# Kernel tuning notes

Hardware: AMD Instinct MI355X
Metric: run time of the kernel (lower is better)

The kernel has to match this reference:

```python
import jax, jax.numpy as jnp
import numpy as np

N, E, G = 100000, 300000, 4096
ND, ED, H, ZI, ZS, NE, L = 64, 16, 256, 128, 128, 8, 3
LAMBDA_GRL = 1.0


def setup_inputs() -> dict:
    key = jax.random.key(0)
    ks = iter(jax.random.split(key, 64))
    def nrm(shape, scale=0.05):
        return jax.random.normal(next(ks), shape, jnp.float32) * scale
    inp = {
        'x': jax.random.normal(next(ks), (N, ND), jnp.float32),
        'edge_index': jax.random.randint(next(ks), (2, E), 0, N),
        'edge_attr': jax.random.normal(next(ks), (E, ED), jnp.float32),
        'batch': jnp.sort(jax.random.randint(next(ks), (N,), 0, G)),
        'node_W': nrm((ND, H)), 'node_b': nrm((H,)),
        'conv_eps': jnp.zeros((L,), jnp.float32),
        'edge_W': nrm((L, ED, H)), 'edge_b': nrm((L, H)),
        'mlp_W1': nrm((L, H, H)), 'mlp_b1': nrm((L, H)),
        'mlp_W2': nrm((L, H, H)), 'mlp_b2': nrm((L, H)),
        'gn_w': jnp.ones((L, H), jnp.float32), 'gn_b': jnp.zeros((L, H), jnp.float32),
        'gn_ms': jnp.ones((L, H), jnp.float32),
        'finv_W1': nrm((H, ZI)), 'finv_b1': nrm((ZI,)),
        'finv_W2': nrm((ZI, ZI)), 'finv_b2': nrm((ZI,)),
        'fspu_W1': nrm((H, ZS)), 'fspu_b1': nrm((ZS,)),
        'fspu_W2': nrm((ZS, ZS)), 'fspu_b2': nrm((ZS,)),
        'pred_W1': nrm((ZI, ZI)), 'pred_b1': nrm((ZI,)),
        'pred_W2': nrm((ZI, 1)), 'pred_b2': nrm((1,)),
        'adv_W1': nrm((ZI, ZI)), 'adv_b1': nrm((ZI,)),
        'adv_W2': nrm((ZI, NE)), 'adv_b2': nrm((NE,)),
    }
    return inp


def _mlp2(h, W1, b1, W2, b2):
    return jax.nn.relu(h @ W1 + b1) @ W2 + b2


def reference(x, edge_index, edge_attr, batch, node_W, node_b, conv_eps,
              edge_W, edge_b, mlp_W1, mlp_b1, mlp_W2, mlp_b2,
              gn_w, gn_b, gn_ms,
              finv_W1, finv_b1, finv_W2, finv_b2,
              fspu_W1, fspu_b1, fspu_W2, fspu_b2,
              pred_W1, pred_b1, pred_W2, pred_b2,
              adv_W1, adv_b1, adv_W2, adv_b2):
    src, dst = edge_index[0], edge_index[1]
    cnt = jax.ops.segment_sum(jnp.ones((N, 1), jnp.float32), batch, num_segments=G)
    cnt = jnp.maximum(cnt, 1.0)
    h = x @ node_W + node_b  # [N,H]
    for l in range(L):
        # GINEConv: sum_j relu(x_j + lin(e_ij))
        e = edge_attr @ edge_W[l] + edge_b[l]            # [E,H]
        m = jax.nn.relu(h[src] + e)                      # [E,H]
        agg = jax.ops.segment_sum(m, dst, num_segments=N)
        h = _mlp2((1.0 + conv_eps[l]) * h + agg, mlp_W1[l], mlp_b1[l], mlp_W2[l], mlp_b2[l])
        # GraphNorm
        mean = jax.ops.segment_sum(h, batch, num_segments=G) / cnt  # [G,H]
        out = h - gn_ms[l] * mean[batch]
        var = jax.ops.segment_sum(out * out, batch, num_segments=G) / cnt
        h = out * jax.lax.rsqrt(var[batch] + 1e-5) * gn_w[l] + gn_b[l]
        h = jax.nn.relu(h)  # dropout is identity at eval
    hg = jax.ops.segment_sum(h, batch, num_segments=G) / cnt  # global_mean_pool [G,H]
    z_inv = _mlp2(hg, finv_W1, finv_b1, finv_W2, finv_b2)
    z_spu = _mlp2(hg, fspu_W1, fspu_b1, fspu_W2, fspu_b2)
    yhat = _mlp2(z_inv, pred_W1, pred_b1, pred_W2, pred_b2)[:, 0]
    # gradient reversal: identity fwd, -lambda on bwd
    grl = jax.lax.stop_gradient(z_inv) * (1.0 + LAMBDA_GRL) - LAMBDA_GRL * z_inv
    envhat = _mlp2(grl, adv_W1, adv_b1, adv_W2, adv_b2)
    return (hg, z_inv, z_spu, yhat, envhat)
```

## Files before the change

kernel.cpp:

```cpp
#include <hip/hip_runtime.h>
#include <hip/hip_bf16.h>

typedef __bf16 bf16_t;
typedef __bf16 bf16x8 __attribute__((ext_vector_type(8)));
typedef __bf16 bf16x4 __attribute__((ext_vector_type(4)));
typedef float  f32x4  __attribute__((ext_vector_type(4)));

static constexpr int N_NODES = 100000;
static constexpr int N_EDGES = 300000;
static constexpr int N_GRAPH = 4096;
static constexpr int H  = 256;
static constexpr int ND = 64;
static constexpr int ZIC = 128;
static constexpr int NE = 8;
static constexpr int SCAN_B = 1024;

__device__ __forceinline__ int clampi(int v, int lo, int hi) {
  return v < lo ? lo : (v > hi ? hi : v);
}

__device__ __forceinline__ void dma16(const bf16_t* g, bf16_t* lds_base) {
  __builtin_amdgcn_global_load_lds(
      (const __attribute__((address_space(1))) void*)g,
      (__attribute__((address_space(3))) void*)lds_base, 16, 0, 0);
}

__global__ void compute_starts_kernel(const int* __restrict__ batch,
                                      int* __restrict__ starts, int N, int G) {
  int i = blockIdx.x * blockDim.x + threadIdx.x;
  if (i >= N) return;
  int b = clampi(batch[i], 0, G - 1);
  if (i == 0) {
    for (int g = 0; g <= b; ++g) starts[g] = 0;
  } else {
    int p = clampi(batch[i - 1], 0, G - 1);
    for (int g = p + 1; g <= b; ++g) starts[g] = i;
  }
  if (i == N - 1) {
    for (int g = b + 1; g <= G; ++g) starts[g] = N;
  }
}

__global__ void zero2_kernel(int* __restrict__ a, int* __restrict__ b, int N) {
  int i = blockIdx.x * blockDim.x + threadIdx.x;
  if (i < N) { a[i] = 0; b[i] = 0; }
}

__global__ void count_deg_kernel(const int* __restrict__ dst, int* __restrict__ counts, int E, int N) {
  int e = blockIdx.x * blockDim.x + threadIdx.x;
  if (e < E) atomicAdd(&counts[clampi(dst[e], 0, N - 1)], 1);
}

__global__ __launch_bounds__(SCAN_B) void scan1_kernel(const int* __restrict__ counts,
                                                       int* __restrict__ offs,
                                                       int* __restrict__ bsum, int N) {
  __shared__ int tmp[SCAN_B];
  int i = blockIdx.x * SCAN_B + threadIdx.x;
  int v = (i < N) ? counts[i] : 0;
  tmp[threadIdx.x] = v;
  __syncthreads();
  for (int d = 1; d < SCAN_B; d <<= 1) {
    int t = (threadIdx.x >= d) ? tmp[threadIdx.x - d] : 0;
    __syncthreads();
    tmp[threadIdx.x] += t;
    __syncthreads();
  }
  if (i < N) offs[i + 1] = tmp[threadIdx.x];
  if (threadIdx.x == SCAN_B - 1) bsum[blockIdx.x] = tmp[SCAN_B - 1];
  if (i == 0) offs[0] = 0;
}

__global__ void scan2_kernel(int* __restrict__ bsum, int nblk) {
  if (blockIdx.x == 0 && threadIdx.x == 0) {
    int run = 0;
    for (int b = 0; b < nblk; ++b) { int v = bsum[b]; bsum[b] = run; run += v; }
  }
}

__global__ __launch_bounds__(SCAN_B) void scan3_kernel(int* __restrict__ offs,
                                                       const int* __restrict__ bsum, int N) {
  int i = blockIdx.x * SCAN_B + threadIdx.x;
  if (i < N) offs[i + 1] += bsum[blockIdx.x];
}

__global__ void fill_scatter_kernel(const int* __restrict__ src, const int* __restrict__ dst,
                                    const float* __restrict__ eattr,
                                    const int* __restrict__ offs, int* __restrict__ cursor,
                                    int* __restrict__ src_srt, bf16_t* __restrict__ eat16,
                                    int E, int N) {
  int e = blockIdx.x * blockDim.x + threadIdx.x;
  if (e >= E) return;
  int d = clampi(dst[e], 0, N - 1);
  int pos = offs[d] + atomicAdd(&cursor[d], 1);
  if ((unsigned)pos >= (unsigned)E) return;
  int s = src[e];
  src_srt[pos] = ((unsigned)s < (unsigned)N_NODES) ? s : 0;
  const float* ea = eattr + (size_t)e * 16;
  union { bf16_t b[16]; uint4 u[2]; } pk;
#pragma unroll
  for (int k = 0; k < 16; ++k) pk.b[k] = (bf16_t)ea[k];
  uint4* dst16 = (uint4*)(eat16 + ((size_t)pos << 4));
  dst16[0] = pk.u[0];
  dst16[1] = pk.u[1];
}

__global__ void build_ewt16_kernel(const float* __restrict__ edge_W,
                                   bf16_t* __restrict__ ewt) {
  int idx = blockIdx.x * blockDim.x + threadIdx.x;
  if (idx >= 3 * 256 * 16) return;
  int l = idx / (256 * 16);
  int rem = idx - l * 256 * 16;
  int n = rem >> 4, k = rem & 15;
  ewt[idx] = (bf16_t)edge_W[(size_t)l * 16 * 256 + k * 256 + n];
}

__global__ void transpose_kernel(const float* __restrict__ W,
                                 bf16_t* __restrict__ Wt, int K, int Nc,
                                 size_t srcStride, size_t dstStride) {
  __shared__ float tile[32][33];
  const float* Wz = W + (size_t)blockIdx.z * srcStride;
  bf16_t* Wtz = Wt + (size_t)blockIdx.z * dstStride;
  int n0 = blockIdx.x * 32, k0 = blockIdx.y * 32;
  int tx = threadIdx.x, ty = threadIdx.y;
  for (int i = ty; i < 32; i += 8)
    tile[i][tx] = Wz[(size_t)(k0 + i) * Nc + n0 + tx];
  __syncthreads();
  for (int i = ty; i < 32; i += 8)
    Wtz[(size_t)(n0 + i) * K + k0 + tx] = (bf16_t)tile[tx][i];
}

__device__ __forceinline__ void load8_to_lds(const bf16_t* p, bool valid, uint4* dst) {
  uint4 v = make_uint4(0u, 0u, 0u, 0u);
  if (valid) v = *(const uint4*)p;
  *dst = v;
}
__device__ __forceinline__ void load8_to_lds(const float* p, bool valid, uint4* dst) {
  float4 f0 = make_float4(0.f, 0.f, 0.f, 0.f), f1 = f0;
  if (valid) { f0 = *(const float4*)p; f1 = *(const float4*)(p + 4); }
  union { bf16_t b[8]; uint4 u; } pk;
  pk.b[0] = (bf16_t)f0.x; pk.b[1] = (bf16_t)f0.y;
  pk.b[2] = (bf16_t)f0.z; pk.b[3] = (bf16_t)f0.w;
  pk.b[4] = (bf16_t)f1.x; pk.b[5] = (bf16_t)f1.y;
  pk.b[6] = (bf16_t)f1.z; pk.b[7] = (bf16_t)f1.w;
  *dst = pk.u;
}

template<int K, bool RELU, bool OUTF32, typename TIN>
__global__ __launch_bounds__(256) void gemm128_kernel(
    const TIN* __restrict__ U, const bf16_t* __restrict__ Wt,
    const float* __restrict__ bias, void* __restrict__ Out, int M, int Nc) {
  constexpr int LDT = 72;
  __shared__ bf16_t Ut[128 * LDT];
  __shared__ bf16_t Wl[128 * LDT];
  const int m0 = blockIdx.x * 128;
  const int n0 = blockIdx.y * 128;
  const int t = threadIdx.x;
  const int lane = t & 63;
  const int wave = t >> 6;
  const int wm = (wave >> 1) * 64;
  const int wn = (wave & 1) * 64;
  const int srow = t >> 1;
  const int sk = (t & 1) * 32;
  const int lr = lane & 15;
  const int lq = lane >> 4;
  const bool aok = (m0 + srow) < M;
  f32x4 acc[4][4] = {};

  for (int k0 = 0; k0 < K; k0 += 64) {
    const TIN* up = U + (size_t)(m0 + srow) * K + k0 + sk;
    const bf16_t* wp = Wt + (size_t)(n0 + srow) * K + k0 + sk;
#pragma unroll
    for (int q = 0; q < 4; ++q) {
      load8_to_lds(up + q * 8, aok, (uint4*)&Ut[srow * LDT + sk + q * 8]);
      load8_to_lds(wp + q * 8, true, (uint4*)&Wl[srow * LDT + sk + q * 8]);
    }
    __syncthreads();
#pragma unroll
    for (int s = 0; s < 2; ++s) {
      bf16x8 a[4], b[4];
#pragma unroll
      for (int mt = 0; mt < 4; ++mt)
        a[mt] = *(const bf16x8*)(&Ut[(wm + mt * 16 + lr) * LDT + s * 32 + lq * 8]);
#pragma unroll
      for (int nt = 0; nt < 4; ++nt)
        b[nt] = *(const bf16x8*)(&Wl[(wn + nt * 16 + lr) * LDT + s * 32 + lq * 8]);
#pragma unroll
      for (int mt = 0; mt < 4; ++mt)
#pragma unroll
        for (int nt = 0; nt < 4; ++nt)
          acc[mt][nt] = __builtin_amdgcn_mfma_f32_16x16x32_bf16(
              a[mt], b[nt], acc[mt][nt], 0, 0, 0);
    }
    __syncthreads();
  }

#pragma unroll
  for (int mt = 0; mt < 4; ++mt)
#pragma unroll
    for (int nt = 0; nt < 4; ++nt) {
      int col = n0 + wn + nt * 16 + lr;
      float bcol = bias[col];
#pragma unroll
      for (int r = 0; r < 4; ++r) {
        int row = m0 + wm + mt * 16 + lq * 4 + r;
        if (row < M) {
          float vv = acc[mt][nt][r] + bcol;
          if (RELU) vv = vv > 0.f ? vv : 0.f;
          if (OUTF32) ((float*)Out)[(size_t)row * Nc + col] = vv;
          else        ((bf16_t*)Out)[(size_t)row * Nc + col] = (bf16_t)vv;
        }
      }
    }
}

template<int K, bool RELU, bool OUTF32, typename TIN>
__global__ __launch_bounds__(256) void gemm64_kernel(
    const TIN* __restrict__ U, const bf16_t* __restrict__ Wt,
    const float* __restrict__ bias, void* __restrict__ Out, int M, int Nc) {
  constexpr int LDT = 72;
  __shared__ bf16_t Ut[64 * LDT];
  __shared__ bf16_t Wl[64 * LDT];
  const int m0 = blockIdx.x * 64;
  const int n0 = blockIdx.y * 64;
  const int t = threadIdx.x;
  const int lane = t & 63;
  const int wave = t >> 6;
  const int wm = (wave >> 1) * 32;
  const int wn = (wave & 1) * 32;
  const int srow = t >> 2;
  const int sk = (t & 3) * 8;
  const int lr = lane & 15;
  const int lq = lane >> 4;
  const bool aok = (m0 + srow) < M;
  f32x4 acc[2][2] = {};

  for (int k0 = 0; k0 < K; k0 += 64) {
    const TIN* up = U + (size_t)(m0 + srow) * K + k0 + sk;
    const bf16_t* wp = Wt + (size_t)(n0 + srow) * K + k0 + sk;
    load8_to_lds(up,      aok, (uint4*)&Ut[srow * LDT + sk]);
    load8_to_lds(up + 32, aok, (uint4*)&Ut[srow * LDT + sk + 32]);
    load8_to_lds(wp,      true, (uint4*)&Wl[srow * LDT + sk]);
    load8_to_lds(wp + 32, true, (uint4*)&Wl[srow * LDT + sk + 32]);
    __syncthreads();
#pragma unroll
    for (int s = 0; s < 2; ++s) {
      bf16x8 a[2], b[2];
#pragma unroll
      for (int mt = 0; mt < 2; ++mt)
        a[mt] = *(const bf16x8*)(&Ut[(wm + mt * 16 + lr) * LDT + s * 32 + lq * 8]);
#pragma unroll
      for (int nt = 0; nt < 2; ++nt)
        b[nt] = *(const bf16x8*)(&Wl[(wn + nt * 16 + lr) * LDT + s * 32 + lq * 8]);
#pragma unroll
      for (int mt = 0; mt < 2; ++mt)
#pragma unroll
        for (int nt = 0; nt < 2; ++nt)
          acc[mt][nt] = __builtin_amdgcn_mfma_f32_16x16x32_bf16(
              a[mt], b[nt], acc[mt][nt], 0, 0, 0);
    }
    __syncthreads();
  }

#pragma unroll
  for (int mt = 0; mt < 2; ++mt)
#pragma unroll
    for (int nt = 0; nt < 2; ++nt) {
      int col = n0 + wn + nt * 16 + lr;
      float bcol = bias[col];
#pragma unroll
      for (int r = 0; r < 4; ++r) {
        int row = m0 + wm + mt * 16 + lq * 4 + r;
        if (row < M) {
          float vv = acc[mt][nt][r] + bcol;
          if (RELU) vv = vv > 0.f ? vv : 0.f;
          if (OUTF32) ((float*)Out)[(size_t)row * Nc + col] = vv;
          else        ((bf16_t*)Out)[(size_t)row * Nc + col] = (bf16_t)vv;
        }
      }
    }
}

template<int K, bool RELU, bool OUTF32>
__global__ __launch_bounds__(256) void gemm128_dma_kernel(
    const bf16_t* __restrict__ U, const bf16_t* __restrict__ Wt,
    const float* __restrict__ bias, void* __restrict__ Out, int M, int Nc) {
  __shared__ bf16_t Ut[128 * 64];
  __shared__ bf16_t Wl[128 * 64];
  const int t = threadIdx.x;
  const int lane = t & 63;
  const int wave = t >> 6;
  const int m0 = blockIdx.x * 128;
  const int n0 = blockIdx.y * 128;
  const int wm = (wave >> 1) * 64;
  const int wn = (wave & 1) * 64;
  const int lr = lane & 15;
  const int lq = lane >> 4;
  const int subrow = wave * 8 + (lane >> 3);
  const int lchunk = (lane & 7) ^ (lane >> 3);
  f32x4 acc[4][4] = {};

  for (int k0 = 0; k0 < K; k0 += 64) {
#pragma unroll
    for (int q = 0; q < 4; ++q) {
      const int row = q * 32 + subrow;
      int urow = m0 + row; if (urow >= M) urow = M - 1;
      dma16(U + (size_t)urow * K + k0 + lchunk * 8, &Ut[(q * 32 + wave * 8) * 64]);
      dma16(Wt + (size_t)(n0 + row) * K + k0 + lchunk * 8, &Wl[(q * 32 + wave * 8) * 64]);
    }
    __syncthreads();
#pragma unroll
    for (int s = 0; s < 2; ++s) {
      bf16x8 a[4], b[4];
#pragma unroll
      for (int mt = 0; mt < 4; ++mt)
        a[mt] = *(const bf16x8*)(&Ut[(wm + mt * 16 + lr) * 64 + (((s * 4 + lq) ^ (lr & 7)) << 3)]);
#pragma unroll
      for (int nt = 0; nt < 4; ++nt)
        b[nt] = *(const bf16x8*)(&Wl[(wn + nt * 16 + lr) * 64 + (((s * 4 + lq) ^ (lr & 7)) << 3)]);
#pragma unroll
      for (int mt = 0; mt < 4; ++mt)
#pragma unroll
        for (int nt = 0; nt < 4; ++nt)
          acc[mt][nt] = __builtin_amdgcn_mfma_f32_16x16x32_bf16(
              a[mt], b[nt], acc[mt][nt], 0, 0, 0);
    }
    __syncthreads();
  }

#pragma unroll
  for (int mt = 0; mt < 4; ++mt)
#pragma unroll
    for (int nt = 0; nt < 4; ++nt) {
      int col = n0 + wn + nt * 16 + lr;
      float bcol = bias[col];
#pragma unroll
      for (int r = 0; r < 4; ++r) {
        int row = m0 + wm + mt * 16 + lq * 4 + r;
        if (row < M) {
          float vv = acc[mt][nt][r] + bcol;
          if (RELU) vv = vv > 0.f ? vv : 0.f;
          if (OUTF32) ((float*)Out)[(size_t)row * Nc + col] = vv;
          else        ((bf16_t*)Out)[(size_t)row * Nc + col] = (bf16_t)vv;
        }
      }
    }
}

__global__ __launch_bounds__(256) void gine_gather_mfma_kernel(
    const bf16_t* __restrict__ h, const bf16_t* __restrict__ eat16,
    const int* __restrict__ src_sorted, const int* __restrict__ offs,
    const bf16_t* __restrict__ ewt, const float* __restrict__ eb,
    const float* __restrict__ eps_p, bf16_t* __restrict__ u) {
  constexpr int HP = H + 8;
  __shared__ bf16_t slin[2][16 * HP];
  const int t = threadIdx.x;
  const int wave = t >> 6;
  const int lane = t & 63;
  const int lr = lane & 15;
  const int lq = lane >> 4;
  const int lane4 = lane * 4;
  const int n0 = blockIdx.x * 4;
  const int nodeN = n0 + wave;

  bf16x4 hs = *(const bf16x4*)(h + (size_t)nodeN * H + lane4);

  bf16x8 bfrag[4];
#pragma unroll
  for (int nt = 0; nt < 4; ++nt) {
    bf16x8 bv = {};
    if (lq < 2)
      bv = *(const bf16x8*)(ewt + ((wave * 64 + nt * 16 + lr) << 4) + (lq << 3));
    bfrag[nt] = bv;
  }
  float ebv[4];
#pragma unroll
  for (int i = 0; i < 4; ++i) ebv[i] = eb[lane4 + i];

  int bs = offs[n0], be = offs[n0 + 4];
  bs = clampi(bs, 0, N_EDGES);
  be = clampi(be, bs, N_EDGES);
  int ns = offs[nodeN], ne = offs[nodeN + 1];
  ns = clampi(ns, bs, be);
  ne = clampi(ne, ns, be);

  float acc[4] = {0.f, 0.f, 0.f, 0.f};
  int parity = 0;

  for (int cb = bs; cb < be; cb += 16, parity ^= 1) {
    int arow = cb + lr;
    if (arow >= N_EDGES) arow = N_EDGES - 1;
    bf16x8 afrag = {};
    if (lq < 2)
      afrag = *(const bf16x8*)(eat16 + ((size_t)arow << 4) + (lq << 3));
    f32x4 c[4];
#pragma unroll
    for (int nt = 0; nt < 4; ++nt) {
      f32x4 z = {};
      c[nt] = __builtin_amdgcn_mfma_f32_16x16x32_bf16(afrag, bfrag[nt], z, 0, 0, 0);
    }
#pragma unroll
    for (int nt = 0; nt < 4; ++nt)
#pragma unroll
      for (int r = 0; r < 4; ++r)
        slin[parity][(lq * 4 + r) * HP + wave * 64 + nt * 16 + lr] = (bf16_t)c[nt][r];
    __syncthreads();
    int j0 = ns > cb ? ns : cb;
    int j1 = ne < cb + 16 ? ne : cb + 16;
    for (int jb = j0; jb < j1; jb += 4) {
      int sidx[4];
#pragma unroll
      for (int q = 0; q < 4; ++q) {
        int jj = jb + q; if (jj > j1 - 1) jj = j1 - 1;
        sidx[q] = src_sorted[jj];
      }
      bf16x4 hv[4];
#pragma unroll
      for (int q = 0; q < 4; ++q)
        hv[q] = *(const bf16x4*)(h + (size_t)sidx[q] * H + lane4);
#pragma unroll
      for (int q = 0; q < 4; ++q) {
        if (jb + q < j1) {
          bf16x4 lv = *(const bf16x4*)(&slin[parity][(jb + q - cb) * HP + lane4]);
#pragma unroll
          for (int i = 0; i < 4; ++i)
            acc[i] += fmaxf((float)hv[q][i] + (float)lv[i] + ebv[i], 0.f);
        }
      }
    }
  }

  const float sc = 1.0f + eps_p[0];
  union { bf16x4 v; uint2 b; } o;
#pragma unroll
  for (int i = 0; i < 4; ++i) o.v[i] = (bf16_t)(sc * (float)hs[i] + acc[i]);
  *(uint2*)(u + (size_t)nodeN * H + lane4) = o.b;
}

__global__ __launch_bounds__(64) void graphnorm_kernel(
    const bf16_t* __restrict__ v, bf16_t* __restrict__ hout,
    const int* __restrict__ starts,
    const float* __restrict__ w, const float* __restrict__ b,
    const float* __restrict__ ms, float* __restrict__ hg) {
  const int g = blockIdx.x;
  const int c0 = threadIdx.x * 4;
  int s = starts[g], e = starts[g + 1];
  s = clampi(s, 0, N_NODES);
  e = clampi(e, s, N_NODES);
  const float cnt = (float)((e - s) > 1 ? (e - s) : 1);
  float sx[4] = {0.f, 0.f, 0.f, 0.f}, sxx[4] = {0.f, 0.f, 0.f, 0.f};
  int i = s;
  for (; i + 4 <= e; i += 4) {
    bf16x4 xv[4];
#pragma unroll
    for (int q = 0; q < 4; ++q)
      xv[q] = *(const bf16x4*)(v + (size_t)(i + q) * H + c0);
#pragma unroll
    for (int q = 0; q < 4; ++q)
#pragma unroll
      for (int j = 0; j < 4; ++j) { float f = (float)xv[q][j]; sx[j] += f; sxx[j] += f * f; }
  }
  for (; i < e; ++i) {
    bf16x4 xv = *(const bf16x4*)(v + (size_t)i * H + c0);
#pragma unroll
    for (int j = 0; j < 4; ++j) { float f = (float)xv[j]; sx[j] += f; sxx[j] += f * f; }
  }
  float sub[4], inv[4], bb[4], psum[4] = {0.f, 0.f, 0.f, 0.f};
#pragma unroll
  for (int j = 0; j < 4; ++j) {
    float mean = sx[j] / cnt;
    sub[j] = ms[c0 + j] * mean;
    float var = sxx[j] / cnt - 2.f * sub[j] * mean + sub[j] * sub[j];
    var = fmaxf(var, 0.f);
    inv[j] = rsqrtf(var + 1e-5f) * w[c0 + j];
    bb[j] = b[c0 + j];
  }
  i = s;
  for (; i + 4 <= e; i += 4) {
    bf16x4 xv[4];
#pragma unroll
    for (int q = 0; q < 4; ++q)
      xv[q] = *(const bf16x4*)(v + (size_t)(i + q) * H + c0);
#pragma unroll
    for (int q = 0; q < 4; ++q) {
      union { bf16x4 o; uint2 u; } pk;
#pragma unroll
      for (int j = 0; j < 4; ++j) {
        float o = ((float)xv[q][j] - sub[j]) * inv[j] + bb[j];
        o = o > 0.f ? o : 0.f;
        psum[j] += o;
        pk.o[j] = (bf16_t)o;
      }
      *(uint2*)(hout + (size_t)(i + q) * H + c0) = pk.u;
    }
  }
  for (; i < e; ++i) {
    bf16x4 xv = *(const bf16x4*)(v + (size_t)i * H + c0);
    union { bf16x4 o; uint2 u; } pk;
#pragma unroll
    for (int j = 0; j < 4; ++j) {
      float o = ((float)xv[j] - sub[j]) * inv[j] + bb[j];
      o = o > 0.f ? o : 0.f;
      psum[j] += o;
      pk.o[j] = (bf16_t)o;
    }
    *(uint2*)(hout + (size_t)i * H + c0) = pk.u;
  }
  if (hg) {
#pragma unroll
    for (int j = 0; j < 4; ++j) hg[(size_t)g * H + c0 + j] = psum[j] / cnt;
  }
}

__global__ void head_out_kernel(const bf16_t* __restrict__ In, const float* __restrict__ W,
                                const float* __restrict__ bias, float* __restrict__ Out,
                                int M, int K, int Nc) {
  int idx = blockIdx.x * blockDim.x + threadIdx.x;
  if (idx >= M * Nc) return;
  int r = idx / Nc, n = idx - r * Nc;
  float acc = bias[n];
  const bf16_t* in = In + (size_t)r * K;
  for (int k = 0; k < K; ++k) acc += (float)in[k] * W[(size_t)k * Nc + n];
  Out[idx] = acc;
}

extern "C" void kernel_launch(void* const* d_in, const int* in_sizes, int n_in,
                              void* d_out, int out_size, void* d_ws, size_t ws_size,
                              hipStream_t stream) {
  (void)in_sizes; (void)n_in; (void)out_size; (void)ws_size;
  const float* x        = (const float*)d_in[0];
  const int*   eidx     = (const int*)d_in[1];
  const float* eattr    = (const float*)d_in[2];
  const int*   batch    = (const int*)d_in[3];
  const float* node_W   = (const float*)d_in[4];
  const float* node_b   = (const float*)d_in[5];
  const float* conv_eps = (const float*)d_in[6];
  const float* edge_W   = (const float*)d_in[7];
  const float* edge_b   = (const float*)d_in[8];
  const float* mlp_W1   = (const float*)d_in[9];
  const float* mlp_b1   = (const float*)d_in[10];
  const float* mlp_W2   = (const float*)d_in[11];
  const float* mlp_b2   = (const float*)d_in[12];
  const float* gn_w     = (const float*)d_in[13];
  const float* gn_b     = (const float*)d_in[14];
  const float* gn_ms    = (const float*)d_in[15];
  const float* finv_W1  = (const float*)d_in[16];
  const float* finv_b1  = (const float*)d_in[17];
  const float* finv_W2  = (const float*)d_in[18];
  const float* finv_b2  = (const float*)d_in[19];
  const float* fspu_W1  = (const float*)d_in[20];
  const float* fspu_b1  = (const float*)d_in[21];
  const float* fspu_W2  = (const float*)d_in[22];
  const float* fspu_b2  = (const float*)d_in[23];
  const float* pred_W1  = (const float*)d_in[24];
  const float* pred_b1  = (const float*)d_in[25];
  const float* pred_W2  = (const float*)d_in[26];
  const float* pred_b2  = (const float*)d_in[27];
  const float* adv_W1   = (const float*)d_in[28];
  const float* adv_b1   = (const float*)d_in[29];
  const float* adv_W2   = (const float*)d_in[30];
  const float* adv_b2   = (const float*)d_in[31];
  float* out = (float*)d_out;

  float* out_hg = out;
  float* out_zi = out + (size_t)N_GRAPH * H;
  float* out_zs = out_zi + (size_t)N_GRAPH * ZIC;
  float* out_yh = out_zs + (size_t)N_GRAPH * ZIC;
  float* out_ev = out_yh + N_GRAPH;

  char* wp = (char*)d_ws;
  auto alloc = [&](size_t bytes) { char* p = wp; wp += (bytes + 255) & ~(size_t)255; return p; };
  bf16_t* A        = (bf16_t*)alloc((size_t)N_NODES * H * 2);
  bf16_t* B        = (bf16_t*)alloc((size_t)N_NODES * H * 2);
  bf16_t* Wt       = (bf16_t*)alloc((size_t)(H * ND + 6 * H * H) * 2);
  bf16_t* WtH      = (bf16_t*)alloc((size_t)(2 * ZIC * H + 4 * ZIC * ZIC) * 2);
  bf16_t* ewt16    = (bf16_t*)alloc((size_t)3 * 256 * 16 * 2);
  bf16_t* eat16    = (bf16_t*)alloc((size_t)N_EDGES * 16 * 2);
  int*    starts   = (int*)alloc((size_t)(N_GRAPH + 1) * 4);
  int*    counts   = (int*)alloc((size_t)N_NODES * 4);
  int*    cursor   = (int*)alloc((size_t)N_NODES * 4);
  int*    offs     = (int*)alloc((size_t)(N_NODES + 1) * 4);
  int*    bsum     = (int*)alloc((size_t)SCAN_B * 4);
  int*    src_srt  = (int*)alloc((size_t)N_EDGES * 4);
  bf16_t* tmp1     = (bf16_t*)alloc((size_t)N_GRAPH * ZIC * 2);
  bf16_t* tmp2     = (bf16_t*)alloc((size_t)N_GRAPH * ZIC * 2);

  const int* srcp = eidx;
  const int* dstp = eidx + N_EDGES;
  const int nscan = (N_NODES + SCAN_B - 1) / SCAN_B;

  compute_starts_kernel<<<(N_NODES + 255) / 256, 256, 0, stream>>>(batch, starts, N_NODES, N_GRAPH);

  zero2_kernel<<<(N_NODES + 255) / 256, 256, 0, stream>>>(counts, cursor, N_NODES);
  count_deg_kernel<<<(N_EDGES + 255) / 256, 256, 0, stream>>>(dstp, counts, N_EDGES, N_NODES);
  scan1_kernel<<<nscan, SCAN_B, 0, stream>>>(counts, offs, bsum, N_NODES);
  scan2_kernel<<<1, 64, 0, stream>>>(bsum, nscan);
  scan3_kernel<<<nscan, SCAN_B, 0, stream>>>(offs, bsum, N_NODES);
  fill_scatter_kernel<<<(N_EDGES + 255) / 256, 256, 0, stream>>>(
      srcp, dstp, eattr, offs, cursor, src_srt, eat16, N_EDGES, N_NODES);
  build_ewt16_kernel<<<(3 * 256 * 16 + 255) / 256, 256, 0, stream>>>(edge_W, ewt16);

  bf16_t* WtN = Wt;
  bf16_t* Wt1base = Wt + H * ND;
  bf16_t* Wt2base = Wt + H * ND + (size_t)H * H;
  auto Wt1l = [&](int l) { return Wt1base + (size_t)(2 * l) * H * H; };
  auto Wt2l = [&](int l) { return Wt2base + (size_t)(2 * l) * H * H; };
  transpose_kernel<<<dim3(H / 32, ND / 32, 1), dim3(32, 8), 0, stream>>>(node_W, WtN, ND, H, 0, 0);
  transpose_kernel<<<dim3(H / 32, H / 32, 3), dim3(32, 8), 0, stream>>>(
      mlp_W1, Wt1base, H, H, (size_t)H * H, (size_t)2 * H * H);
  transpose_kernel<<<dim3(H / 32, H / 32, 3), dim3(32, 8), 0, stream>>>(
      mlp_W2, Wt2base, H, H, (size_t)H * H, (size_t)2 * H * H);

  bf16_t* fT1 = WtH;
  bf16_t* fT2 = fT1 + ZIC * H;
  bf16_t* sT1 = fT2 + ZIC * ZIC;
  bf16_t* sT2 = sT1 + ZIC * H;
  bf16_t* pT1 = sT2 + ZIC * ZIC;
  bf16_t* aT1 = pT1 + ZIC * ZIC;
  transpose_kernel<<<dim3(ZIC / 32, H / 32, 1), dim3(32, 8), 0, stream>>>(finv_W1, fT1, H, ZIC, 0, 0);
  transpose_kernel<<<dim3(ZIC / 32, ZIC / 32, 1), dim3(32, 8), 0, stream>>>(finv_W2, fT2, ZIC, ZIC, 0, 0);
  transpose_kernel<<<dim3(ZIC / 32, H / 32, 1), dim3(32, 8), 0, stream>>>(fspu_W1, sT1, H, ZIC, 0, 0);
  transpose_kernel<<<dim3(ZIC / 32, ZIC / 32, 1), dim3(32, 8), 0, stream>>>(fspu_W2, sT2, ZIC, ZIC, 0, 0);
  transpose_kernel<<<dim3(ZIC / 32, ZIC / 32, 1), dim3(32, 8), 0, stream>>>(pred_W1, pT1, ZIC, ZIC, 0, 0);
  transpose_kernel<<<dim3(ZIC / 32, ZIC / 32, 1), dim3(32, 8), 0, stream>>>(adv_W1, aT1, ZIC, ZIC, 0, 0);

  dim3 ggrid((N_NODES + 127) / 128, H / 128);
  gemm128_kernel<ND, false, false><<<ggrid, 256, 0, stream>>>(x, WtN, node_b, A, N_NODES, H);

  for (int l = 0; l < 3; ++l) {
    gine_gather_mfma_kernel<<<N_NODES / 4, 256, 0, stream>>>(
        A, eat16, src_srt, offs, ewt16 + (size_t)l * 256 * 16,
        edge_b + l * H, conv_eps + l, B);
    gemm128_dma_kernel<H, true,  false><<<ggrid, 256, 0, stream>>>(B, Wt1l(l), mlp_b1 + l * H, A, N_NODES, H);
    gemm128_dma_kernel<H, false, false><<<ggrid, 256, 0, stream>>>(A, Wt2l(l), mlp_b2 + l * H, B, N_NODES, H);
    graphnorm_kernel<<<N_GRAPH, 64, 0, stream>>>(B, A, starts, gn_w + l * H, gn_b + l * H,
                                                 gn_ms + l * H, (l == 2) ? out_hg : nullptr);
  }

  dim3 hgrid(N_GRAPH / 64, ZIC / 64);
  gemm64_kernel<H,   true,  false, float ><<<hgrid, 256, 0, stream>>>(out_hg, fT1, finv_b1, tmp1, N_GRAPH, ZIC);
  gemm64_kernel<ZIC, false, true,  bf16_t><<<hgrid, 256, 0, stream>>>(tmp1, fT2, finv_b2, out_zi, N_GRAPH, ZIC);
  gemm64_kernel<H,   true,  false, float ><<<hgrid, 256, 0, stream>>>(out_hg, sT1, fspu_b1, tmp2, N_GRAPH, ZIC);
  gemm64_kernel<ZIC, false, true,  bf16_t><<<hgrid, 256, 0, stream>>>(tmp2, sT2, fspu_b2, out_zs, N_GRAPH, ZIC);
  gemm64_kernel<ZIC, true,  false, float ><<<hgrid, 256, 0, stream>>>(out_zi, pT1, pred_b1, tmp1, N_GRAPH, ZIC);
  gemm64_kernel<ZIC, true,  false, float ><<<hgrid, 256, 0, stream>>>(out_zi, aT1, adv_b1, tmp2, N_GRAPH, ZIC);
  head_out_kernel<<<(N_GRAPH + 255) / 256, 256, 0, stream>>>(tmp1, pred_W2, pred_b2, out_yh, N_GRAPH, ZIC, 1);
  head_out_kernel<<<(N_GRAPH * NE + 255) / 256, 256, 0, stream>>>(tmp2, adv_W2, adv_b2, out_ev, N_GRAPH, ZIC, NE);
}
```

Measured before the change: 822.0 us.

## Widen graphnorm to four waves, batch head GEMMs, fold edge bias into MFMA

```diff
diff --git a/kernel.cpp b/kernel.cpp
--- a/kernel.cpp
+++ b/kernel.cpp
@@ -214,12 +214,18 @@
 }
 
 template<int K, bool RELU, bool OUTF32, typename TIN>
-__global__ __launch_bounds__(256) void gemm64_kernel(
-    const TIN* __restrict__ U, const bf16_t* __restrict__ Wt,
-    const float* __restrict__ bias, void* __restrict__ Out, int M, int Nc) {
+__global__ __launch_bounds__(256) void gemm64x2_kernel(
+    const TIN* __restrict__ U0, const bf16_t* __restrict__ Wt0,
+    const float* __restrict__ b0, void* __restrict__ O0,
+    const TIN* __restrict__ U1, const bf16_t* __restrict__ Wt1,
+    const float* __restrict__ b1, void* __restrict__ O1, int M, int Nc) {
   constexpr int LDT = 72;
   __shared__ bf16_t Ut[64 * LDT];
   __shared__ bf16_t Wl[64 * LDT];
+  const TIN*    U    = blockIdx.z ? U1 : U0;
+  const bf16_t* Wt   = blockIdx.z ? Wt1 : Wt0;
+  const float*  bias = blockIdx.z ? b1 : b0;
+  void*         Out  = blockIdx.z ? O1 : O0;
   const int m0 = blockIdx.x * 64;
   const int n0 = blockIdx.y * 64;
   const int t = threadIdx.x;
@@ -365,16 +371,16 @@
   bf16x4 hs = *(const bf16x4*)(h + (size_t)nodeN * H + lane4);
 
   bf16x8 bfrag[4];
+  f32x4 zb[4];
 #pragma unroll
   for (int nt = 0; nt < 4; ++nt) {
     bf16x8 bv = {};
     if (lq < 2)
       bv = *(const bf16x8*)(ewt + ((wave * 64 + nt * 16 + lr) << 4) + (lq << 3));
     bfrag[nt] = bv;
-  }
-  float ebv[4];
-#pragma unroll
-  for (int i = 0; i < 4; ++i) ebv[i] = eb[lane4 + i];
+    float ebw = eb[wave * 64 + nt * 16 + lr];
+    zb[nt][0] = ebw; zb[nt][1] = ebw; zb[nt][2] = ebw; zb[nt][3] = ebw;
+  }
 
   int bs = offs[n0], be = offs[n0 + 4];
   bs = clampi(bs, 0, N_EDGES);
@@ -394,10 +400,8 @@
       afrag = *(const bf16x8*)(eat16 + ((size_t)arow << 4) + (lq << 3));
     f32x4 c[4];
 #pragma unroll
-    for (int nt = 0; nt < 4; ++nt) {
-      f32x4 z = {};
-      c[nt] = __builtin_amdgcn_mfma_f32_16x16x32_bf16(afrag, bfrag[nt], z, 0, 0, 0);
-    }
+    for (int nt = 0; nt < 4; ++nt)
+      c[nt] = __builtin_amdgcn_mfma_f32_16x16x32_bf16(afrag, bfrag[nt], zb[nt], 0, 0, 0);
 #pragma unroll
     for (int nt = 0; nt < 4; ++nt)
 #pragma unroll
@@ -423,7 +427,7 @@
           bf16x4 lv = *(const bf16x4*)(&slin[parity][(jb + q - cb) * HP + lane4]);
 #pragma unroll
           for (int i = 0; i < 4; ++i)
-            acc[i] += fmaxf((float)hv[q][i] + (float)lv[i] + ebv[i], 0.f);
+            acc[i] += fmaxf((float)hv[q][i] + (float)lv[i], 0.f);
         }
       }
     }
@@ -436,91 +440,144 @@
   *(uint2*)(u + (size_t)nodeN * H + lane4) = o.b;
 }
 
-__global__ __launch_bounds__(64) void graphnorm_kernel(
+__global__ __launch_bounds__(256) void graphnorm_kernel(
     const bf16_t* __restrict__ v, bf16_t* __restrict__ hout,
     const int* __restrict__ starts,
     const float* __restrict__ w, const float* __restrict__ b,
     const float* __restrict__ ms, float* __restrict__ hg) {
+  constexpr int RS = 9;
+  constexpr int PS = 13;
+  __shared__ float red[4 * 64 * RS];
+  __shared__ float prm[64 * PS];
   const int g = blockIdx.x;
-  const int c0 = threadIdx.x * 4;
+  const int t = threadIdx.x;
+  const int lane = t & 63;
+  const int wave = t >> 6;
+  const int c0 = lane * 4;
   int s = starts[g], e = starts[g + 1];
   s = clampi(s, 0, N_NODES);
   e = clampi(e, s, N_NODES);
   const float cnt = (float)((e - s) > 1 ? (e - s) : 1);
+
   float sx[4] = {0.f, 0.f, 0.f, 0.f}, sxx[4] = {0.f, 0.f, 0.f, 0.f};
-  int i = s;
-  for (; i + 4 <= e; i += 4) {
-    bf16x4 xv[4];
-#pragma unroll
-    for (int q = 0; q < 4; ++q)
-      xv[q] = *(const bf16x4*)(v + (size_t)(i + q) * H + c0);
-#pragma unroll
-    for (int q = 0; q < 4; ++q)
-#pragma unroll
-      for (int j = 0; j < 4; ++j) { float f = (float)xv[q][j]; sx[j] += f; sxx[j] += f * f; }
-  }
-  for (; i < e; ++i) {
-    bf16x4 xv = *(const bf16x4*)(v + (size_t)i * H + c0);
-#pragma unroll
-    for (int j = 0; j < 4; ++j) { float f = (float)xv[j]; sx[j] += f; sxx[j] += f * f; }
-  }
-  float sub[4], inv[4], bb[4], psum[4] = {0.f, 0.f, 0.f, 0.f};
+  {
+    int i = s + wave;
+    for (; i + 4 < e; i += 8) {
+      bf16x4 x0 = *(const bf16x4*)(v + (size_t)i * H + c0);
+      bf16x4 x1 = *(const bf16x4*)(v + (size_t)(i + 4) * H + c0);
+#pragma unroll
+      for (int j = 0; j < 4; ++j) {
+        float f0 = (float)x0[j], f1 = (float)x1[j];
+        sx[j] += f0 + f1; sxx[j] += f0 * f0 + f1 * f1;
+      }
+    }
+    if (i < e) {
+      bf16x4 x0 = *(const bf16x4*)(v + (size_t)i * H + c0);
+#pragma unroll
+      for (int j = 0; j < 4; ++j) {
+        float f0 = (float)x0[j];
+        sx[j] += f0; sxx[j] += f0 * f0;
+      }
+    }
+  }
+  float* myred = &red[(wave * 64 + lane) * RS];
+#pragma unroll
+  for (int j = 0; j < 4; ++j) { myred[j] = sx[j]; myred[4 + j] = sxx[j]; }
+  __syncthreads();
+
+  if (wave == 0) {
+#pragma unroll
+    for (int j = 0; j < 4; ++j) {
+      float fsx = red[lane * RS + j] + red[(64 + lane) * RS + j] +
+                  red[(128 + lane) * RS + j] + red[(192 + lane) * RS + j];
+      float fsxx = red[lane * RS + 4 + j] + red[(64 + lane) * RS + 4 + j] +
+                   red[(128 + lane) * RS + 4 + j] + red[(192 + lane) * RS + 4 + j];
+      float mean = fsx / cnt;
+      float sub = ms[c0 + j] * mean;
+      float var = fsxx / cnt - 2.f * sub * mean + sub * sub;
+      var = fmaxf(var, 0.f);
+      prm[lane * PS + j] = sub;
+      prm[lane * PS + 4 + j] = rsqrtf(var + 1e-5f) * w[c0 + j];
+      prm[lane * PS + 8 + j] = b[c0 + j];
+    }
+  }
+  __syncthreads();
+  float sub[4], inv[4], bb[4];
 #pragma unroll
   for (int j = 0; j < 4; ++j) {
-    float mean = sx[j] / cnt;
-    sub[j] = ms[c0 + j] * mean;
-    float var = sxx[j] / cnt - 2.f * sub[j] * mean + sub[j] * sub[j];
-    var = fmaxf(var, 0.f);
-    inv[j] = rsqrtf(var + 1e-5f) * w[c0 + j];
-    bb[j] = b[c0 + j];
-  }
-  i = s;
-  for (; i + 4 <= e; i += 4) {
-    bf16x4 xv[4];
-#pragma unroll
-    for (int q = 0; q < 4; ++q)
-      xv[q] = *(const bf16x4*)(v + (size_t)(i + q) * H + c0);
-#pragma unroll
-    for (int q = 0; q < 4; ++q) {
-      union { bf16x4 o; uint2 u; } pk;
+    sub[j] = prm[lane * PS + j];
+    inv[j] = prm[lane * PS + 4 + j];
+    bb[j] = prm[lane * PS + 8 + j];
+  }
+
+  float psum[4] = {0.f, 0.f, 0.f, 0.f};
+  {
+    int i = s + wave;
+    for (; i + 4 < e; i += 8) {
+      bf16x4 x0 = *(const bf16x4*)(v + (size_t)i * H + c0);
+      bf16x4 x1 = *(const bf16x4*)(v + (size_t)(i + 4) * H + c0);
+      union { bf16x4 o; uint2 u; } p0, p1;
 #pragma unroll
       for (int j = 0; j < 4; ++j) {
-        float o = ((float)xv[q][j] - sub[j]) * inv[j] + bb[j];
-        o = o > 0.f ? o : 0.f;
-        psum[j] += o;
-        pk.o[j] = (bf16_t)o;
-      }
-      *(uint2*)(hout + (size_t)(i + q) * H + c0) = pk.u;
-    }
-  }
-  for (; i < e; ++i) {
-    bf16x4 xv = *(const bf16x4*)(v + (size_t)i * H + c0);
-    union { bf16x4 o; uint2 u; } pk;
-#pragma unroll
-    for (int j = 0; j < 4; ++j) {
-      float o = ((float)xv[j] - sub[j]) * inv[j] + bb[j];
-      o = o > 0.f ? o : 0.f;
-      psum[j] += o;
-      pk.o[j] = (bf16_t)o;
-    }
-    *(uint2*)(hout + (size_t)i * H + c0) = pk.u;
-  }
+        float o0 = ((float)x0[j] - sub[j]) * inv[j] + bb[j];
+        float o1 = ((float)x1[j] - sub[j]) * inv[j] + bb[j];
+        o0 = o0 > 0.f ? o0 : 0.f;
+        o1 = o1 > 0.f ? o1 : 0.f;
+        psum[j] += o0 + o1;
+        p0.o[j] = (bf16_t)o0; p1.o[j] = (bf16_t)o1;
+      }
+      *(uint2*)(hout + (size_t)i * H + c0) = p0.u;
+      *(uint2*)(hout + (size_t)(i + 4) * H + c0) = p1.u;
+    }
+    if (i < e) {
+      bf16x4 x0 = *(const bf16x4*)(v + (size_t)i * H + c0);
+      union { bf16x4 o; uint2 u; } p0;
+#pragma unroll
+      for (int j = 0; j < 4; ++j) {
+        float o0 = ((float)x0[j] - sub[j]) * inv[j] + bb[j];
+        o0 = o0 > 0.f ? o0 : 0.f;
+        psum[j] += o0;
+        p0.o[j] = (bf16_t)o0;
+      }
+      *(uint2*)(hout + (size_t)i * H + c0) = p0.u;
+    }
+  }
+
   if (hg) {
 #pragma unroll
-    for (int j = 0; j < 4; ++j) hg[(size_t)g * H + c0 + j] = psum[j] / cnt;
-  }
-}
-
-__global__ void head_out_kernel(const bf16_t* __restrict__ In, const float* __restrict__ W,
-                                const float* __restrict__ bias, float* __restrict__ Out,
-                                int M, int K, int Nc) {
+    for (int j = 0; j < 4; ++j) myred[j] = psum[j];
+    __syncthreads();
+    if (wave == 0) {
+#pragma unroll
+      for (int j = 0; j < 4; ++j) {
+        float p = red[lane * RS + j] + red[(64 + lane) * RS + j] +
+                  red[(128 + lane) * RS + j] + red[(192 + lane) * RS + j];
+        hg[(size_t)g * H + c0 + j] = p / cnt;
+      }
+    }
+  }
+}
+
+__global__ void head_out2_kernel(const bf16_t* __restrict__ In1, const float* __restrict__ W1,
+                                 const float* __restrict__ b1, float* __restrict__ O1,
+                                 const bf16_t* __restrict__ In2, const float* __restrict__ W2,
+                                 const float* __restrict__ b2, float* __restrict__ O2,
+                                 int M) {
   int idx = blockIdx.x * blockDim.x + threadIdx.x;
-  if (idx >= M * Nc) return;
-  int r = idx / Nc, n = idx - r * Nc;
-  float acc = bias[n];
-  const bf16_t* in = In + (size_t)r * K;
-  for (int k = 0; k < K; ++k) acc += (float)in[k] * W[(size_t)k * Nc + n];
-  Out[idx] = acc;
+  if (idx < M) {
+    float acc = b1[0];
+    const bf16_t* in = In1 + (size_t)idx * ZIC;
+    for (int k = 0; k < ZIC; ++k) acc += (float)in[k] * W1[k];
+    O1[idx] = acc;
+  } else {
+    int j = idx - M;
+    if (j >= M * NE) return;
+    int r = j >> 3, n = j & 7;
+    float acc = b2[n];
+    const bf16_t* in = In2 + (size_t)r * ZIC;
+    for (int k = 0; k < ZIC; ++k) acc += (float)in[k] * W2[(size_t)k * NE + n];
+    O2[j] = acc;
+  }
 }
 
 extern "C" void kernel_launch(void* const* d_in, const int* in_sizes, int n_in,
@@ -632,17 +689,17 @@
         edge_b + l * H, conv_eps + l, B);
     gemm128_dma_kernel<H, true,  false><<<ggrid, 256, 0, stream>>>(B, Wt1l(l), mlp_b1 + l * H, A, N_NODES, H);
     gemm128_dma_kernel<H, false, false><<<ggrid, 256, 0, stream>>>(A, Wt2l(l), mlp_b2 + l * H, B, N_NODES, H);
-    graphnorm_kernel<<<N_GRAPH, 64, 0, stream>>>(B, A, starts, gn_w + l * H, gn_b + l * H,
-                                                 gn_ms + l * H, (l == 2) ? out_hg : nullptr);
-  }
-
-  dim3 hgrid(N_GRAPH / 64, ZIC / 64);
-  gemm64_kernel<H,   true,  false, float ><<<hgrid, 256, 0, stream>>>(out_hg, fT1, finv_b1, tmp1, N_GRAPH, ZIC);
-  gemm64_kernel<ZIC, false, true,  bf16_t><<<hgrid, 256, 0, stream>>>(tmp1, fT2, finv_b2, out_zi, N_GRAPH, ZIC);
-  gemm64_kernel<H,   true,  false, float ><<<hgrid, 256, 0, stream>>>(out_hg, sT1, fspu_b1, tmp2, N_GRAPH, ZIC);
-  gemm64_kernel<ZIC, false, true,  bf16_t><<<hgrid, 256, 0, stream>>>(tmp2, sT2, fspu_b2, out_zs, N_GRAPH, ZIC);
-  gemm64_kernel<ZIC, true,  false, float ><<<hgrid, 256, 0, stream>>>(out_zi, pT1, pred_b1, tmp1, N_GRAPH, ZIC);
-  gemm64_kernel<ZIC, true,  false, float ><<<hgrid, 256, 0, stream>>>(out_zi, aT1, adv_b1, tmp2, N_GRAPH, ZIC);
-  head_out_kernel<<<(N_GRAPH + 255) / 256, 256, 0, stream>>>(tmp1, pred_W2, pred_b2, out_yh, N_GRAPH, ZIC, 1);
-  head_out_kernel<<<(N_GRAPH * NE + 255) / 256, 256, 0, stream>>>(tmp2, adv_W2, adv_b2, out_ev, N_GRAPH, ZIC, NE);
-}
+    graphnorm_kernel<<<N_GRAPH, 256, 0, stream>>>(B, A, starts, gn_w + l * H, gn_b + l * H,
+                                                  gn_ms + l * H, (l == 2) ? out_hg : nullptr);
+  }
+
+  dim3 hgrid2(N_GRAPH / 64, ZIC / 64, 2);
+  gemm64x2_kernel<H, true, false, float><<<hgrid2, 256, 0, stream>>>(
+      out_hg, fT1, finv_b1, tmp1, out_hg, sT1, fspu_b1, tmp2, N_GRAPH, ZIC);
+  gemm64x2_kernel<ZIC, false, true, bf16_t><<<hgrid2, 256, 0, stream>>>(
+      tmp1, fT2, finv_b2, out_zi, tmp2, sT2, fspu_b2, out_zs, N_GRAPH, ZIC);
+  gemm64x2_kernel<ZIC, true, false, float><<<hgrid2, 256, 0, stream>>>(
+      out_zi, pT1, pred_b1, tmp1, out_zi, aT1, adv_b1, tmp2, N_GRAPH, ZIC);
+  head_out2_kernel<<<(N_GRAPH * (1 + NE) + 255) / 256, 256, 0, stream>>>(
+      tmp1, pred_W2, pred_b2, out_yh, tmp2, adv_W2, adv_b2, out_ev, N_GRAPH);
+}
```

Measured after the change: 795.2 us. 3.3% less time.
